# Kernel tuning notes

Hardware: AMD Instinct MI355X
Metric: run time of the kernel (lower is better)

## Reference

```python
import math
import jax, jax.numpy as jnp
import numpy as np

# ---- static config (from init_kwargs) ----
B = 4
FH, FW = 480, 640          # frame size
NSEM = 16
C_OBS = 4 + NSEM           # 20 obs channels (rgb, depth, sem)
C_FEAT = 1 + NSEM          # 17 splatted feature channels
RES = 5.0                  # map resolution cm
VR = 100                   # vision range (cells)
MAXH, MINH = 72, -8        # int(360/5), int(-40/5)
HZ = MAXH - MINH           # 80 height bins
MAP_CELLS = 480            # (4800//2)//5
AGENT_H = 88.0             # camera_height*100
FOV = 79.0
N = FH * FW                # du_scale = 1
MAP_T, EXP_T, CAT_T = 1.0, 1.0, 5.0
DEG = 57.29577951308232
MIN_Z, MAX_Z = 13, 25      # int(25/5 - min_h), int((agent_h+1)/5 - min_h)
X1, X2 = 190, 290          # map crop window
Y1, Y2 = 240, 340


def setup_inputs() -> dict:
    key = jax.random.key(0)
    k1, k2, k3, k4, k5 = jax.random.split(key, 5)
    obs = jax.random.uniform(k1, (B, C_OBS, FH, FW), jnp.float32)
    obs = obs.at[:, 3].multiply(500.0)  # depth channel in cm
    pose_obs = jax.random.normal(k2, (B, 3), jnp.float32) * 0.1
    maps_last = jax.random.uniform(k3, (B, C_OBS, MAP_CELLS, MAP_CELLS), jnp.float32)
    poses_last = jax.random.normal(k4, (B, 3), jnp.float32) * 0.3 \
        + jnp.array([12.0, 12.0, 0.0], jnp.float32)  # near map center (meters, deg)
    sh = jax.random.normal(k5, (B, N, 4), jnp.float32) * 0.1  # SH coeffs per point
    return {"obs": obs, "pose_obs": pose_obs, "maps_last": maps_last,
            "poses_last": poses_last, "sh": sh}


def _affine_grid(theta, H, W):
    # align_corners=True affine grid; theta: (bs, 2, 3) -> (bs, H, W, 2)
    ys = jnp.linspace(-1.0, 1.0, H, dtype=jnp.float32)
    xs = jnp.linspace(-1.0, 1.0, W, dtype=jnp.float32)
    gx, gy = jnp.meshgrid(xs, ys)                       # (H, W)
    base = jnp.stack([gx, gy, jnp.ones_like(gx)], -1)   # (H, W, 3)
    return jnp.einsum('bij,hwj->bhwi', theta, base)


def _grid_sample(img, grid):
    # bilinear, zeros padding, align_corners=True. img: (bs,C,H,W), grid: (bs,H,W,2)
    Bs, C, H, W = img.shape
    x = (grid[..., 0] + 1.0) * (W - 1) / 2.0
    y = (grid[..., 1] + 1.0) * (H - 1) / 2.0
    x0 = jnp.floor(x); y0 = jnp.floor(y)
    x1 = x0 + 1.0; y1 = y0 + 1.0

    def one(img_b, xb, yb, x0b, y0b, x1b, y1b):
        def tap(ix, iy):
            valid = ((ix >= 0) & (ix < W) & (iy >= 0) & (iy < H)).astype(img_b.dtype)
            ic = jnp.clip(ix, 0, W - 1).astype(jnp.int32)
            jc = jnp.clip(iy, 0, H - 1).astype(jnp.int32)
            return img_b[:, jc, ic] * valid[None]        # (C,H,W)
        w00 = (x1b - xb) * (y1b - yb)
        w01 = (xb - x0b) * (y1b - yb)
        w10 = (x1b - xb) * (yb - y0b)
        w11 = (xb - x0b) * (yb - y0b)
        return (tap(x0b, y0b) * w00[None] + tap(x1b, y0b) * w01[None]
                + tap(x0b, y1b) * w10[None] + tap(x1b, y1b) * w11[None])

    return jax.vmap(one)(img, x, y, x0, y0, x1, y1)


def _splat_one(feat_b, coords_b):
    # trilinear scatter-add splat (du.splat_feat_nd). feat_b: (C_FEAT, N), coords_b: (3, N) in [-1,1]
    GD = (VR, VR, HZ)
    grid = jnp.zeros((C_FEAT, VR * VR * HZ), jnp.float32)
    pos = [coords_b[d] * GD[d] / 2.0 + GD[d] / 2.0 for d in range(3)]
    for ix in ((0, 0, 0), (0, 0, 1), (0, 1, 0), (0, 1, 1),
               (1, 0, 0), (1, 0, 1), (1, 1, 0), (1, 1, 1)):
        idx = jnp.zeros((N,), jnp.float32)
        w = jnp.ones((N,), jnp.float32)
        for d in range(3):
            p = jnp.floor(pos[d]) + ix[d]
            safe = ((p > 0) & (p < GD[d])).astype(jnp.float32)
            w = w * (1.0 - jnp.abs(pos[d] - p)) * safe
            idx = idx * GD[d] + p * safe
        grid = grid.at[:, idx.astype(jnp.int32)].add(feat_b * w[None, :])
    return grid


def _forward(obs, pose_obs, maps_last, poses_last, sh):
    bs = obs.shape[0]
    depth = obs[:, 3]                                   # (bs, FH, FW)

    # --- point cloud from depth (du.get_point_cloud_from_z_t) ---
    f = (FW / 2.0) / math.tan(math.radians(FOV / 2.0))
    xc = (FW - 1) / 2.0
    zc = (FH - 1) / 2.0
    gx = jnp.arange(FW, dtype=jnp.float32)
    gz = jnp.arange(FH - 1, -1, -1, dtype=jnp.float32)
    X = (gx[None, None, :] - xc) * depth / f
    Z = (gz[None, :, None] - zc) * depth / f
    # camera view transform (elev=0 -> identity rot, z += agent_h) then
    # shift_loc pose transform (angle pi/2 -> identity rot, x += vr*res//2)
    x_s = X + float(VR * int(RES) // 2)
    y_s = depth
    z_s = Z + AGENT_H

    # --- normalize to [-1,1] voxel coords ---
    xn = (x_s / RES - float(VR // 2)) / VR * 2.0
    yn = (y_s / RES - float(VR // 2)) / VR * 2.0
    zn = (z_s / RES - float((MAXH + MINH) // 2)) / (MAXH - MINH) * 2.0
    coords = jnp.stack([xn, yn, zn], axis=1).reshape(bs, 3, N)
    coords = jnp.clip(coords, -1.0, 1.0)

    # --- features (channel 0 = ones occupancy, rest = semantics; du_scale=1 so avgpool is identity) ---
    feat = jnp.concatenate(
        [jnp.ones((bs, 1, N), jnp.float32), obs[:, 4:].reshape(bs, NSEM, N)], axis=1)
    sh_mean = jnp.mean(sh, axis=2)                      # (bs, N)
    enh = feat * (1.0 + sh_mean[:, None, :])

    # --- voxel splat + round, swap the two xy grid dims (matches .transpose(2,3)) ---
    vox = jax.vmap(_splat_one)(enh, coords)
    vox = jnp.round(vox).reshape(bs, C_FEAT, VR, VR, HZ).transpose(0, 1, 3, 2, 4)

    # --- height projections ---
    agent_proj = vox[..., MIN_Z:MAX_Z].sum(-1)          # (bs, C_FEAT, VR, VR)
    all_proj = vox.sum(-1)
    fp_map_pred = jnp.clip(agent_proj[:, 0:1] / MAP_T, 0.0, 1.0)
    fp_exp_pred = jnp.clip(all_proj[:, 0:1] / EXP_T, 0.0, 1.0)

    # --- write into egocentric map ---
    av = jnp.zeros((bs, C_OBS, MAP_CELLS, MAP_CELLS), jnp.float32)
    av = av.at[:, 0:1, Y1:Y2, X1:X2].set(fp_map_pred)
    av = av.at[:, 1:2, Y1:Y2, X1:X2].set(fp_exp_pred)
    av = av.at[:, 4:, Y1:Y2, X1:X2].set(jnp.clip(agent_proj[:, 1:] / CAT_T, 0.0, 1.0))

    # --- pose integration ---
    t0 = poses_last[:, 2] / DEG
    y_new = poses_last[:, 1] + pose_obs[:, 0] * jnp.sin(t0) + pose_obs[:, 1] * jnp.cos(t0)
    x_new = poses_last[:, 0] + pose_obs[:, 0] * jnp.cos(t0) - pose_obs[:, 1] * jnp.sin(t0)
    t_new = poses_last[:, 2] + pose_obs[:, 2] * DEG
    t_new = jnp.fmod(t_new - 180.0, 360.0) + 180.0
    t_new = jnp.fmod(t_new + 180.0, 360.0) - 180.0
    current_poses = jnp.stack([x_new, y_new, t_new], axis=1)

    # --- spatial transform of egocentric map into allocentric frame ---
    stc = jax.lax.stop_gradient(current_poses)          # matches .clone().detach()
    half = float(MAP_CELLS // 2)                        # 240
    st_xy = -(stc[:, :2] * 100.0 / RES - half) / half
    st_t = (90.0 - stc[:, 2]) * (math.pi / 180.0)
    cos_t, sin_t = jnp.cos(st_t), jnp.sin(st_t)
    zeros = jnp.zeros_like(cos_t); ones = jnp.ones_like(cos_t)
    theta1 = jnp.stack([jnp.stack([cos_t, -sin_t, zeros], 1),
                        jnp.stack([sin_t, cos_t, zeros], 1)], 1)    # (bs,2,3)
    theta2 = jnp.stack([jnp.stack([ones, zeros, st_xy[:, 0]], 1),
                        jnp.stack([zeros, ones, st_xy[:, 1]], 1)], 1)
    rot_grid = _affine_grid(theta1, MAP_CELLS, MAP_CELLS)
    trans_grid = _affine_grid(theta2, MAP_CELLS, MAP_CELLS)
    rotated = _grid_sample(av, rot_grid)
    translated = _grid_sample(rotated, trans_grid)

    map_pred = jnp.maximum(maps_last, translated)
    # pose_pred aliases poses_last which is mutated in-place in torch -> equals current_poses
    return fp_map_pred, map_pred, current_poses, current_poses


def reference(obs, pose_obs, maps_last, poses_last, sh):
    return _forward(obs, pose_obs, maps_last, poses_last, sh)
```

## Files before the change

kernel.cpp:

```cpp
#include <hip/hip_runtime.h>
#include <math.h>

#define FHh 480
#define FWw 640
#define NPIX (FHh*FWw)
#define NSEMC 16
#define COBS 20
#define MAPC 480
#define VRc 100
#define HZc 80
#define MINZc 13
#define MAXZc 25
#define ZW 12
#define NB 4
#define NBINS_DIM 101
#define NBINS_ROW 101
#define NBINS_TOTAL (NB*NBINS_DIM*NBINS_ROW)
#define COUNTS_PAD 40960

__global__ void pose_kernel(const float* __restrict__ pose_obs,
                            const float* __restrict__ poses_last,
                            float* __restrict__ out_p1,
                            float* __restrict__ out_p2,
                            float* __restrict__ params)
{
    int b = threadIdx.x;
    if (b >= NB) return;
    float pl0 = poses_last[b*3+0], pl1 = poses_last[b*3+1], pl2 = poses_last[b*3+2];
    float po0 = pose_obs[b*3+0],  po1 = pose_obs[b*3+1],  po2 = pose_obs[b*3+2];
    const float DEGf = 57.29577951308232f;
    float t0 = pl2 / DEGf;
    float s = sinf(t0), c = cosf(t0);
    float y_new = pl1 + po0*s + po1*c;
    float x_new = pl0 + po0*c - po1*s;
    float t_new = pl2 + po2*DEGf;
    t_new = fmodf(t_new - 180.0f, 360.0f) + 180.0f;
    t_new = fmodf(t_new + 180.0f, 360.0f) - 180.0f;
    out_p1[b*3+0]=x_new; out_p1[b*3+1]=y_new; out_p1[b*3+2]=t_new;
    out_p2[b*3+0]=x_new; out_p2[b*3+1]=y_new; out_p2[b*3+2]=t_new;
    float sx = -(((x_new*100.0f)/5.0f - 240.0f)/240.0f);
    float sy = -(((y_new*100.0f)/5.0f - 240.0f)/240.0f);
    float st_t = (90.0f - t_new) * 0.017453292519943295f;
    params[b*4+0] = cosf(st_t);
    params[b*4+1] = sinf(st_t);
    params[b*4+2] = sx;
    params[b*4+3] = sy;
}

__device__ __forceinline__ float4 pixel_pos(const float* __restrict__ obsb,
                                            const float* __restrict__ sh,
                                            int b, int n, float fconst)
{
    int col = n % FWw, row = n / FWw;
    float depth = obsb[3*NPIX + n];
    const float4 s4 = ((const float4*)sh)[(size_t)b*NPIX + n];
    float sm = (((s4.x + s4.y) + s4.z) + s4.w) / 4.0f;
    float factor = 1.0f + sm;

    float X = ((float)col - 319.5f) * depth / fconst;
    float Z = ((float)(FHh-1-row) - 239.5f) * depth / fconst;
    float x_s = X + 250.0f;
    float z_s = Z + 88.0f;
    float xn = (x_s/5.0f - 50.0f)/100.0f*2.0f;
    float yn = (depth/5.0f - 50.0f)/100.0f*2.0f;
    float zn = (z_s/5.0f - 32.0f)/80.0f*2.0f;
    xn = fminf(fmaxf(xn,-1.0f),1.0f);
    yn = fminf(fmaxf(yn,-1.0f),1.0f);
    zn = fminf(fmaxf(zn,-1.0f),1.0f);
    float pos0 = (xn*100.0f)/2.0f + 50.0f;
    float pos1 = (yn*100.0f)/2.0f + 50.0f;
    float pos2 = (zn*80.0f)/2.0f + 40.0f;
    return make_float4(pos0, pos1, pos2, factor);
}

__global__ void bin_count_kernel(const float* __restrict__ obs,
                                 const float* __restrict__ sh,
                                 float4* __restrict__ tmpPos,
                                 int* __restrict__ auxBid,
                                 int* __restrict__ auxRank,
                                 int* __restrict__ counts,
                                 float fconst)
{
    int g = blockIdx.x*blockDim.x + threadIdx.x;
    if (g >= NB*NPIX) return;
    int b = g / NPIX, n = g % NPIX;
    const float* obsb = obs + (size_t)b*COBS*NPIX;
    float4 P = pixel_pos(obsb, sh, b, n, fconst);
    int f0 = (int)floorf(P.x); if (f0 > 100) f0 = 100;
    int f1 = (int)floorf(P.y); if (f1 > 100) f1 = 100;
    int bid = (b*NBINS_DIM + f0)*NBINS_ROW + f1;
    int r = atomicAdd(&counts[bid], 1);
    tmpPos[g] = P;
    auxBid[g] = bid;
    auxRank[g] = r;
}

__global__ void scan_kernel(int* __restrict__ counts)
{
    __shared__ int part[1024];
    int t = threadIdx.x;
    const int CHUNK = COUNTS_PAD / 1024;
    int base = t*CHUNK;
    int s = 0;
    for (int k = 0; k < CHUNK; ++k) s += counts[base+k];
    part[t] = s;
    __syncthreads();
    for (int off = 1; off < 1024; off <<= 1) {
        int v = (t >= off) ? part[t-off] : 0;
        __syncthreads();
        part[t] += v;
        __syncthreads();
    }
    int run = part[t] - s;
    for (int k = 0; k < CHUNK; ++k) {
        int c = counts[base+k];
        counts[base+k] = run;
        run += c;
    }
}

__global__ void scatter_kernel(const float4* __restrict__ tmpPos,
                               const int* __restrict__ auxBid,
                               const int* __restrict__ auxRank,
                               const int* __restrict__ offsets,
                               float4* __restrict__ payloadPos,
                               int* __restrict__ payloadN)
{
    int g = blockIdx.x*blockDim.x + threadIdx.x;
    if (g >= NB*NPIX) return;
    int dst = offsets[auxBid[g]] + auxRank[g];
    payloadPos[dst] = tmpPos[g];
    payloadN[dst] = g % NPIX;
}

__global__ __launch_bounds__(128)
void gather_kernel(const float* __restrict__ obs,
                   const float4* __restrict__ payloadPos,
                   const int* __restrict__ payloadN,
                   const int* __restrict__ offsets,
                   float* __restrict__ avwin,
                   float* __restrict__ fp_out)
{
    int cell = blockIdx.x;
    int b = blockIdx.y;
    int tid = threadIdx.x;
    int i = cell % VRc, j = cell / VRc;

    __shared__ float acc[HZc + NSEMC*ZW];
    for (int k = tid; k < HZc + NSEMC*ZW; k += 128) acc[k] = 0.0f;
    __syncthreads();

    if (i > 0 && j > 0) {
        const float* obsb = obs + (size_t)b*COBS*NPIX;
        #pragma unroll
        for (int fi = 0; fi < 2; ++fi) {
            int f0r = i - 1 + fi;
            int rb = (b*NBINS_DIM + f0r)*NBINS_ROW;
            int s = offsets[rb + j - 1];
            int e = offsets[rb + j + 1];
            for (int idx = s + tid; idx < e; idx += 128) {
                float4 P = payloadPos[idx];
                float wx = 1.0f - fabsf(P.x - (float)i);
                float wy = 1.0f - fabsf(P.y - (float)j);
                float wxy = wx * wy;
                if (wxy <= 0.0f) continue;
                float f2 = floorf(P.z);
                float wsem0 = 0.0f, wsem1 = 0.0f;
                int qA = (int)f2, qB = qA + 1;
                if (qA > 0 && qA < HZc) {
                    float w = wxy * (1.0f - fabsf(P.z - (float)qA));
                    if (w > 0.0f) {
                        atomicAdd(&acc[qA], P.w * w);
                        if (qA >= MINZc && qA < MAXZc) wsem0 = w;
                    }
                }
                if (qB > 0 && qB < HZc) {
                    float w = wxy * (1.0f - fabsf(P.z - (float)qB));
                    if (w > 0.0f) {
                        atomicAdd(&acc[qB], P.w * w);
                        if (qB >= MINZc && qB < MAXZc) wsem1 = w;
                    }
                }
                if (wsem0 > 0.0f || wsem1 > 0.0f) {
                    int n = payloadN[idx];
                    int zA = qA - MINZc, zB = qB - MINZc;
                    #pragma unroll
                    for (int c = 0; c < NSEMC; ++c) {
                        float enh = obsb[(4+c)*NPIX + n] * P.w;
                        if (wsem0 > 0.0f) atomicAdd(&acc[HZc + c*ZW + zA], enh * wsem0);
                        if (wsem1 > 0.0f) atomicAdd(&acc[HZc + c*ZW + zB], enh * wsem1);
                    }
                }
            }
        }
    }
    __syncthreads();

    float* avb = avwin + (size_t)b*18*10000;
    if (tid < NSEMC) {
        float sum = 0.0f;
        #pragma unroll
        for (int z = 0; z < ZW; ++z) sum += rintf(acc[HZc + tid*ZW + z]);
        avb[(2+tid)*10000 + cell] = fminf(fmaxf(sum/5.0f, 0.0f), 1.0f);
    } else if (tid == 16) {
        float agent = 0.0f;
        #pragma unroll
        for (int z = MINZc; z < MAXZc; ++z) agent += rintf(acc[z]);
        float v = fminf(fmaxf(agent, 0.0f), 1.0f);
        avb[0*10000 + cell] = v;
        fp_out[(size_t)b*10000 + cell] = v;
    } else if (tid == 17) {
        float all = 0.0f;
        for (int z = 0; z < HZc; ++z) all += rintf(acc[z]);
        avb[1*10000 + cell] = fminf(fmaxf(all, 0.0f), 1.0f);
    }
}

__device__ __forceinline__ float grid1d(int i) {
    return (float)(-1.0 + (double)i * (2.0/479.0));
}

__global__ void map_kernel(const float* __restrict__ maps_last,
                           const float* __restrict__ avwin,
                           const float* __restrict__ params,
                           float* __restrict__ map_out)
{
    int t = blockIdx.x*blockDim.x + threadIdx.x;
    if (t >= NB*MAPC*MAPC) return;
    int w = t % MAPC;
    int h = (t / MAPC) % MAPC;
    int b = t / (MAPC*MAPC);
    float ct = params[b*4+0], st = params[b*4+1];
    float sx = params[b*4+2], sy = params[b*4+3];

    float xg = grid1d(w) + sx;
    float yg = grid1d(h) + sy;
    float xt = ((xg + 1.0f)*479.0f)/2.0f;
    float yt = ((yg + 1.0f)*479.0f)/2.0f;
    float xf = floorf(xt), yf = floorf(yt);

    float acc[18];
    #pragma unroll
    for (int k=0;k<18;k++) acc[k]=0.0f;
    const float* avb = avwin + (size_t)b*18*10000;

    #pragma unroll
    for (int oy=0; oy<2; ++oy) {
        #pragma unroll
        for (int ox=0; ox<2; ++ox) {
            float qx = xf + (float)ox, qy = yf + (float)oy;
            if (!(qx >= 0.0f && qx < 480.0f && qy >= 0.0f && qy < 480.0f)) continue;
            float wo = (ox ? (xt - xf) : (xf + 1.0f - xt))
                     * (oy ? (yt - yf) : (yf + 1.0f - yt));
            int oxi = (int)qx, oyi = (int)qy;
            float gxr = grid1d(oxi), gyr = grid1d(oyi);
            float xr = ct*gxr - st*gyr;
            float yr = st*gxr + ct*gyr;
            float xp = ((xr + 1.0f)*479.0f)/2.0f;
            float yp = ((yr + 1.0f)*479.0f)/2.0f;
            float xpf = floorf(xp), ypf = floorf(yp);
            float R[18];
            #pragma unroll
            for (int k=0;k<18;k++) R[k]=0.0f;
            #pragma unroll
            for (int iy=0; iy<2; ++iy) {
                #pragma unroll
                for (int ix=0; ix<2; ++ix) {
                    float rx = xpf + (float)ix, ry = ypf + (float)iy;
                    if (!(rx >= 0.0f && rx < 480.0f && ry >= 0.0f && ry < 480.0f)) continue;
                    int rxi = (int)rx, ryi = (int)ry;
                    if (ryi < 240 || ryi >= 340 || rxi < 190 || rxi >= 290) continue;
                    float wi = (ix ? (xp - xpf) : (xpf + 1.0f - xp))
                             * (iy ? (yp - ypf) : (yp + 1.0f - yp - (yp - ypf)));
                    wi = (ix ? (xp - xpf) : (xpf + 1.0f - xp))
                       * (iy ? (yp - ypf) : (ypf + 1.0f - yp));
                    const float* p = avb + (ryi-240)*VRc + (rxi-190);
                    #pragma unroll
                    for (int k=0;k<18;k++) R[k] += wi * p[k*10000];
                }
            }
            #pragma unroll
            for (int k=0;k<18;k++) acc[k] += wo * R[k];
        }
    }

    #pragma unroll
    for (int c=0;c<COBS;c++) {
        size_t o = (((size_t)b*COBS + c)*MAPC + h)*MAPC + w;
        float tv = (c==0) ? acc[0] : (c==1) ? acc[1] : (c>=4) ? acc[c-2] : 0.0f;
        map_out[o] = fmaxf(maps_last[o], tv);
    }
}

extern "C" void kernel_launch(void* const* d_in, const int* in_sizes, int n_in,
                              void* d_out, int out_size, void* d_ws, size_t ws_size,
                              hipStream_t stream)
{
    const float* obs        = (const float*)d_in[0];
    const float* pose_obs   = (const float*)d_in[1];
    const float* maps_last  = (const float*)d_in[2];
    const float* poses_last = (const float*)d_in[3];
    const float* sh         = (const float*)d_in[4];
    float* out = (float*)d_out;

    float* fp_out  = out;
    float* map_out = out + 40000;
    float* poses1  = out + 40000 + 18432000;
    float* poses2  = poses1 + 12;

    float* params = (float*)d_ws;
    float* avwin  = params + 16;

    const int NTOT = NB*NPIX;
    float4* tmpPos     = (float4*)map_out;
    float4* payloadPos = (float4*)(map_out + 4915200);
    int*    auxBid     = (int*)(map_out + 9830400);
    int*    auxRank    = (int*)(map_out + 11059200);
    int*    payloadN   = (int*)(map_out + 12288000);
    int*    counts     = (int*)(map_out + 13516800);

    double rad = 39.5 * 0.017453292519943295;
    float fconst = (float)(320.0 / tan(rad));

    hipLaunchKernelGGL(pose_kernel, dim3(1), dim3(64), 0, stream,
                       pose_obs, poses_last, poses1, poses2, params);

    hipMemsetAsync(counts, 0, (size_t)COUNTS_PAD*sizeof(int), stream);

    hipLaunchKernelGGL(bin_count_kernel, dim3((NTOT+255)/256), dim3(256), 0, stream,
                       obs, sh, tmpPos, auxBid, auxRank, counts, fconst);

    hipLaunchKernelGGL(scan_kernel, dim3(1), dim3(1024), 0, stream, counts);

    hipLaunchKernelGGL(scatter_kernel, dim3((NTOT+255)/256), dim3(256), 0, stream,
                       tmpPos, auxBid, auxRank, counts, payloadPos, payloadN);

    hipLaunchKernelGGL(gather_kernel, dim3(10000, NB), dim3(128), 0, stream,
                       obs, payloadPos, payloadN, counts, avwin, fp_out);

    hipLaunchKernelGGL(map_kernel, dim3((NB*MAPC*MAPC+255)/256), dim3(256), 0, stream,
                       maps_last, avwin, params, map_out);
}
```

Baseline: 812.7 us.

## Cull out-of-range points and pre-pack semantic band payload for gather

```diff
diff --git a/kernel.cpp b/kernel.cpp
--- a/kernel.cpp
+++ b/kernel.cpp
@@ -15,8 +15,9 @@
 #define NB 4
 #define NBINS_DIM 101
 #define NBINS_ROW 101
-#define NBINS_TOTAL (NB*NBINS_DIM*NBINS_ROW)
 #define COUNTS_PAD 40960
+#define BANDMAX 600000
+#define NTOT (NB*NPIX)
 
 __global__ void pose_kernel(const float* __restrict__ pose_obs,
                             const float* __restrict__ poses_last,
@@ -73,36 +74,50 @@
     return make_float4(pos0, pos1, pos2, factor);
 }
 
+__device__ __forceinline__ bool dim_ok(float p, int GD)
+{
+    int f = (int)floorf(p);
+    float fr = p - (float)f;
+    bool t0 = (f > 0) && (f < GD);
+    bool t1 = (f + 1 < GD) && (fr > 0.0f);
+    return t0 || t1;
+}
+
 __global__ void bin_count_kernel(const float* __restrict__ obs,
                                  const float* __restrict__ sh,
-                                 float4* __restrict__ tmpPos,
                                  int* __restrict__ auxBid,
-                                 int* __restrict__ auxRank,
                                  int* __restrict__ counts,
+                                 int* __restrict__ countsB,
                                  float fconst)
 {
     int g = blockIdx.x*blockDim.x + threadIdx.x;
-    if (g >= NB*NPIX) return;
+    if (g >= NTOT) return;
     int b = g / NPIX, n = g % NPIX;
     const float* obsb = obs + (size_t)b*COBS*NPIX;
     float4 P = pixel_pos(obsb, sh, b, n, fconst);
-    int f0 = (int)floorf(P.x); if (f0 > 100) f0 = 100;
-    int f1 = (int)floorf(P.y); if (f1 > 100) f1 = 100;
+
+    bool ok = dim_ok(P.x, VRc) && dim_ok(P.y, VRc) && dim_ok(P.z, HZc);
+    if (!ok) { auxBid[g] = -1; return; }
+
+    int f0 = (int)floorf(P.x);
+    int f1 = (int)floorf(P.y);
     int bid = (b*NBINS_DIM + f0)*NBINS_ROW + f1;
-    int r = atomicAdd(&counts[bid], 1);
-    tmpPos[g] = P;
-    auxBid[g] = bid;
-    auxRank[g] = r;
-}
-
-__global__ void scan_kernel(int* __restrict__ counts)
-{
+    atomicAdd(&counts[bid], 1);
+    bool band = (P.z > 12.0f) && (P.z < 25.0f);
+    if (band) atomicAdd(&countsB[bid], 1);
+    auxBid[g] = band ? (bid | (1<<30)) : bid;
+}
+
+__global__ void scan_kernel(int* __restrict__ base)
+{
+    int* cnt = base + (size_t)blockIdx.x * 2 * COUNTS_PAD;
+    int* wrk = cnt + COUNTS_PAD;
     __shared__ int part[1024];
     int t = threadIdx.x;
     const int CHUNK = COUNTS_PAD / 1024;
-    int base = t*CHUNK;
+    int bo = t*CHUNK;
     int s = 0;
-    for (int k = 0; k < CHUNK; ++k) s += counts[base+k];
+    for (int k = 0; k < CHUNK; ++k) s += cnt[bo+k];
     part[t] = s;
     __syncthreads();
     for (int off = 1; off < 1024; off <<= 1) {
@@ -113,31 +128,61 @@
     }
     int run = part[t] - s;
     for (int k = 0; k < CHUNK; ++k) {
-        int c = counts[base+k];
-        counts[base+k] = run;
+        int c = cnt[bo+k];
+        cnt[bo+k] = run;
+        wrk[bo+k] = run;
         run += c;
     }
 }
 
-__global__ void scatter_kernel(const float4* __restrict__ tmpPos,
+__global__ void scatter_kernel(const float* __restrict__ obs,
+                               const float* __restrict__ sh,
                                const int* __restrict__ auxBid,
-                               const int* __restrict__ auxRank,
-                               const int* __restrict__ offsets,
+                               int* __restrict__ offsetsWork,
+                               int* __restrict__ offsetsWorkB,
                                float4* __restrict__ payloadPos,
-                               int* __restrict__ payloadN)
+                               float4* __restrict__ bandPos,
+                               float4* __restrict__ bandSem,
+                               float fconst)
 {
     int g = blockIdx.x*blockDim.x + threadIdx.x;
-    if (g >= NB*NPIX) return;
-    int dst = offsets[auxBid[g]] + auxRank[g];
-    payloadPos[dst] = tmpPos[g];
-    payloadN[dst] = g % NPIX;
+    if (g >= NTOT) return;
+    int v = auxBid[g];
+    if (v < 0) return;
+    int bid  = v & 0x3FFFFFFF;
+    bool band = (v >> 30) & 1;
+
+    int b = g / NPIX, n = g % NPIX;
+    const float* obsb = obs + (size_t)b*COBS*NPIX;
+    float4 P = pixel_pos(obsb, sh, b, n, fconst);
+
+    int dst = atomicAdd(&offsetsWork[bid], 1);
+    payloadPos[dst] = P;
+
+    if (band) {
+        int dstB = atomicAdd(&offsetsWorkB[bid], 1);
+        if (dstB < BANDMAX) {
+            bandPos[dstB] = P;
+            float4* bs = bandSem + (size_t)dstB*4;
+            #pragma unroll
+            for (int q = 0; q < 4; ++q) {
+                float4 e;
+                e.x = obsb[(4 + 4*q + 0)*NPIX + n] * P.w;
+                e.y = obsb[(4 + 4*q + 1)*NPIX + n] * P.w;
+                e.z = obsb[(4 + 4*q + 2)*NPIX + n] * P.w;
+                e.w = obsb[(4 + 4*q + 3)*NPIX + n] * P.w;
+                bs[q] = e;
+            }
+        }
+    }
 }
 
 __global__ __launch_bounds__(128)
-void gather_kernel(const float* __restrict__ obs,
-                   const float4* __restrict__ payloadPos,
-                   const int* __restrict__ payloadN,
+void gather_kernel(const float4* __restrict__ payloadPos,
                    const int* __restrict__ offsets,
+                   const float4* __restrict__ bandPos,
+                   const float4* __restrict__ bandSem,
+                   const int* __restrict__ offsetsB,
                    float* __restrict__ avwin,
                    float* __restrict__ fp_out)
 {
@@ -151,7 +196,6 @@
     __syncthreads();
 
     if (i > 0 && j > 0) {
-        const float* obsb = obs + (size_t)b*COBS*NPIX;
         #pragma unroll
         for (int fi = 0; fi < 2; ++fi) {
             int f0r = i - 1 + fi;
@@ -164,32 +208,47 @@
                 float wy = 1.0f - fabsf(P.y - (float)j);
                 float wxy = wx * wy;
                 if (wxy <= 0.0f) continue;
-                float f2 = floorf(P.z);
-                float wsem0 = 0.0f, wsem1 = 0.0f;
-                int qA = (int)f2, qB = qA + 1;
+                int qA = (int)floorf(P.z), qB = qA + 1;
+                float fz = P.z - (float)qA;
                 if (qA > 0 && qA < HZc) {
-                    float w = wxy * (1.0f - fabsf(P.z - (float)qA));
-                    if (w > 0.0f) {
-                        atomicAdd(&acc[qA], P.w * w);
-                        if (qA >= MINZc && qA < MAXZc) wsem0 = w;
-                    }
+                    float w = wxy * (1.0f - fz);
+                    if (w > 0.0f) atomicAdd(&acc[qA], P.w * w);
                 }
                 if (qB > 0 && qB < HZc) {
-                    float w = wxy * (1.0f - fabsf(P.z - (float)qB));
-                    if (w > 0.0f) {
-                        atomicAdd(&acc[qB], P.w * w);
-                        if (qB >= MINZc && qB < MAXZc) wsem1 = w;
-                    }
+                    float w = wxy * fz;
+                    if (w > 0.0f) atomicAdd(&acc[qB], P.w * w);
                 }
-                if (wsem0 > 0.0f || wsem1 > 0.0f) {
-                    int n = payloadN[idx];
-                    int zA = qA - MINZc, zB = qB - MINZc;
+            }
+            int sB = offsetsB[rb + j - 1];
+            int eB = offsetsB[rb + j + 1];
+            for (int idx = sB + tid; idx < eB; idx += 128) {
+                float4 P = bandPos[idx];
+                float wx = 1.0f - fabsf(P.x - (float)i);
+                float wy = 1.0f - fabsf(P.y - (float)j);
+                float wxy = wx * wy;
+                if (wxy <= 0.0f) continue;
+                int qA = (int)floorf(P.z), qB = qA + 1;
+                float fz = P.z - (float)qA;
+                float w0 = (qA >= MINZc && qA < MAXZc) ? wxy * (1.0f - fz) : 0.0f;
+                float w1 = (qB >= MINZc && qB < MAXZc) ? wxy * fz          : 0.0f;
+                if (w0 <= 0.0f && w1 <= 0.0f) continue;
+                float4 s0 = bandSem[(size_t)idx*4 + 0];
+                float4 s1 = bandSem[(size_t)idx*4 + 1];
+                float4 s2 = bandSem[(size_t)idx*4 + 2];
+                float4 s3 = bandSem[(size_t)idx*4 + 3];
+                float ev[16] = { s0.x,s0.y,s0.z,s0.w, s1.x,s1.y,s1.z,s1.w,
+                                 s2.x,s2.y,s2.z,s2.w, s3.x,s3.y,s3.z,s3.w };
+                if (w0 > 0.0f) {
+                    int zA = qA - MINZc;
                     #pragma unroll
-                    for (int c = 0; c < NSEMC; ++c) {
-                        float enh = obsb[(4+c)*NPIX + n] * P.w;
-                        if (wsem0 > 0.0f) atomicAdd(&acc[HZc + c*ZW + zA], enh * wsem0);
-                        if (wsem1 > 0.0f) atomicAdd(&acc[HZc + c*ZW + zB], enh * wsem1);
-                    }
+                    for (int c = 0; c < NSEMC; ++c)
+                        atomicAdd(&acc[HZc + c*ZW + zA], ev[c] * w0);
+                }
+                if (w1 > 0.0f) {
+                    int zB = qB - MINZc;
+                    #pragma unroll
+                    for (int c = 0; c < NSEMC; ++c)
+                        atomicAdd(&acc[HZc + c*ZW + zB], ev[c] * w1);
                 }
             }
         }
@@ -271,9 +330,7 @@
                     int rxi = (int)rx, ryi = (int)ry;
                     if (ryi < 240 || ryi >= 340 || rxi < 190 || rxi >= 290) continue;
                     float wi = (ix ? (xp - xpf) : (xpf + 1.0f - xp))
-                             * (iy ? (yp - ypf) : (yp + 1.0f - yp - (yp - ypf)));
-                    wi = (ix ? (xp - xpf) : (xpf + 1.0f - xp))
-                       * (iy ? (yp - ypf) : (ypf + 1.0f - yp));
+                             * (iy ? (yp - ypf) : (ypf + 1.0f - yp));
                     const float* p = avb + (ryi-240)*VRc + (rxi-190);
                     #pragma unroll
                     for (int k=0;k<18;k++) R[k] += wi * p[k*10000];
@@ -311,13 +368,14 @@
     float* params = (float*)d_ws;
     float* avwin  = params + 16;
 
-    const int NTOT = NB*NPIX;
-    float4* tmpPos     = (float4*)map_out;
-    float4* payloadPos = (float4*)(map_out + 4915200);
-    int*    auxBid     = (int*)(map_out + 9830400);
-    int*    auxRank    = (int*)(map_out + 11059200);
-    int*    payloadN   = (int*)(map_out + 12288000);
-    int*    counts     = (int*)(map_out + 13516800);
+    float4* payloadPos  = (float4*)map_out;
+    int*    auxBid      = (int*)(map_out + 4915200);
+    int*    counts      = (int*)(map_out + 6144000);
+    int*    offsetsWork = counts + COUNTS_PAD;
+    int*    countsB     = counts + 2*COUNTS_PAD;
+    int*    offsetsWorkB= counts + 3*COUNTS_PAD;
+    float4* bandPos     = (float4*)(map_out + 6144000 + 4*COUNTS_PAD);
+    float4* bandSem     = (float4*)(map_out + 6144000 + 4*COUNTS_PAD + (size_t)BANDMAX*4);
 
     double rad = 39.5 * 0.017453292519943295;
     float fconst = (float)(320.0 / tan(rad));
@@ -325,18 +383,19 @@
     hipLaunchKernelGGL(pose_kernel, dim3(1), dim3(64), 0, stream,
                        pose_obs, poses_last, poses1, poses2, params);
 
-    hipMemsetAsync(counts, 0, (size_t)COUNTS_PAD*sizeof(int), stream);
+    hipMemsetAsync(counts, 0, (size_t)4*COUNTS_PAD*sizeof(int), stream);
 
     hipLaunchKernelGGL(bin_count_kernel, dim3((NTOT+255)/256), dim3(256), 0, stream,
-                       obs, sh, tmpPos, auxBid, auxRank, counts, fconst);
-
-    hipLaunchKernelGGL(scan_kernel, dim3(1), dim3(1024), 0, stream, counts);
+                       obs, sh, auxBid, counts, countsB, fconst);
+
+    hipLaunchKernelGGL(scan_kernel, dim3(2), dim3(1024), 0, stream, counts);
 
     hipLaunchKernelGGL(scatter_kernel, dim3((NTOT+255)/256), dim3(256), 0, stream,
-                       tmpPos, auxBid, auxRank, counts, payloadPos, payloadN);
+                       obs, sh, auxBid, offsetsWork, offsetsWorkB,
+                       payloadPos, bandPos, bandSem, fconst);
 
     hipLaunchKernelGGL(gather_kernel, dim3(10000, NB), dim3(128), 0, stream,
-                       obs, payloadPos, payloadN, counts, avwin, fp_out);
+                       payloadPos, counts, bandPos, bandSem, countsB, avwin, fp_out);
 
     hipLaunchKernelGGL(map_kernel, dim3((NB*MAPC*MAPC+255)/256), dim3(256), 0, stream,
                        maps_last, avwin, params, map_out);
```

After: 859.9 us. 5.8% more time.
